# Optimization experiments

Hardware: AMD Instinct MI355X
Metric: run time of the kernel (lower is better)

The kernel has to match this reference:

```python
import jax, jax.numpy as jnp
import numpy as np

L, B, T, I, H, O = 2, 64, 256, 512, 1024, 256
HIDDEN_WEIGHT = 0.5  # placement_weight = 1 - hidden_weight
# dropout is identity in eval mode (reference is deterministic)


def setup_inputs() -> dict:
    key = jax.random.key(0)
    ks = jax.random.split(key, 20)
    def unif(k, shape, fan):
        b = 1.0 / np.sqrt(fan)
        return jax.random.uniform(k, shape, jnp.float32, -b, b)
    lengths = jax.random.randint(ks[4], (B,), 0, T + 1)
    lengths = lengths.at[0].set(T).at[1].set(0)  # exercise full-length and zero-length paths
    return {
        "step_input": jax.random.normal(ks[0], (B, T, I), jnp.float32),
        "clstm_hidden": jax.random.normal(ks[1], (B, H), jnp.float32),
        "hidden": jax.random.normal(ks[2], (L, B, H), jnp.float32),
        "cell": jax.random.normal(ks[3], (L, B, H), jnp.float32),
        "input_lengths": lengths.astype(jnp.int64),
        # LSTM params, PyTorch gate order [i, f, g, o]
        "w_ih0": unif(ks[5], (4 * H, I), H), "w_hh0": unif(ks[6], (4 * H, H), H),
        "b_ih0": unif(ks[7], (4 * H,), H), "b_hh0": unif(ks[8], (4 * H,), H),
        "w_ih1": unif(ks[9], (4 * H, H), H), "w_hh1": unif(ks[10], (4 * H, H), H),
        "b_ih1": unif(ks[11], (4 * H,), H), "b_hh1": unif(ks[12], (4 * H,), H),
        "w1": unif(ks[13], (H, H), H), "b1": unif(ks[14], (H,), H),
        "w2": unif(ks[15], (O, H), H), "b2": unif(ks[16], (O,), H),
    }


def compute_weighted_hidden(clstm_hidden, hidden, lens):
    # vectorized version of the per-(layer,batch) min-max rescale loop
    cmin = jnp.min(clstm_hidden, axis=-1, keepdims=True)            # [B,1]
    crange = jnp.max(clstm_hidden, axis=-1, keepdims=True) - cmin   # [B,1]
    safe_cr = jnp.where(crange > 0, crange, 1.0)
    s = jnp.where(crange > 0, (clstm_hidden - cmin) / safe_cr, clstm_hidden)  # [B,H]
    hmin = jnp.min(hidden, axis=-1, keepdims=True)                  # [L,B,1]
    hrange = jnp.max(hidden, axis=-1, keepdims=True) - hmin         # [L,B,1]
    s2 = jnp.where(hrange > 0, hmin + s[None] * hrange,
                   jnp.broadcast_to(s[None], hidden.shape))         # [L,B,H]
    c = jnp.where((lens == 0)[None, :, None], clstm_hidden[None], s2)
    return HIDDEN_WEIGHT * hidden + (1.0 - HIDDEN_WEIGHT) * c


def lstm_forward(x, h0, c0, lens, layer_params):
    # x: [B,T,I]; h0,c0: [L,B,H]; lens already clamped to >=1
    t_idx = jnp.arange(x.shape[1])

    def step(carry, xt_t):
        h, c = carry                      # each [L,B,H]
        xt, t = xt_t                      # xt: [B,I]
        valid = (t < lens)[:, None]       # [B,1]
        inp = xt
        hs, cs = [], []
        for l, (wih, whh, bih, bhh) in enumerate(layer_params):
            gates = inp @ wih.T + bih + h[l] @ whh.T + bhh   # [B,4H]
            i, f, g, o = jnp.split(gates, 4, axis=-1)
            i, f, o = jax.nn.sigmoid(i), jax.nn.sigmoid(f), jax.nn.sigmoid(o)
            g = jnp.tanh(g)
            c_new = f * c[l] + i * g
            h_new = o * jnp.tanh(c_new)
            hs.append(jnp.where(valid, h_new, h[l]))
            cs.append(jnp.where(valid, c_new, c[l]))
            inp = jnp.where(valid, h_new, 0.0)
        out_t = inp                        # top layer output, zeroed on padding
        return (jnp.stack(hs), jnp.stack(cs)), out_t

    (hn, cn), outs = jax.lax.scan(step, (h0, c0), (x.transpose(1, 0, 2), t_idx))
    return outs.transpose(1, 0, 2), hn, cn  # [B,T,H], [L,B,H], [L,B,H]


def reference(step_input, clstm_hidden, hidden, cell, input_lengths,
              w_ih0, w_hh0, b_ih0, b_hh0, w_ih1, w_hh1, b_ih1, b_hh1,
              w1, b1, w2, b2):
    weighted_hidden = compute_weighted_hidden(clstm_hidden, hidden, input_lengths)
    lens = jnp.clip(input_lengths, 1, None)  # torch.clamp(min=1)
    layer_params = [(w_ih0, w_hh0, b_ih0, b_hh0), (w_ih1, w_hh1, b_ih1, b_hh1)]
    lstm_out, hn, cn = lstm_forward(step_input, weighted_hidden, cell, lens, layer_params)
    # dropout layers are identity in eval mode
    h1 = jax.nn.relu(lstm_out @ w1.T + b1)
    logits = jax.nn.relu(h1 @ w2.T + b2)  # [B,T,O]
    zero = (input_lengths == 0)
    logits = jnp.where(zero[:, None, None], 0.0, logits)
    hn = jnp.where(zero[None, :, None], 0.0, hn)
    cn = jnp.where(zero[None, :, None], 0.0, cn)
    return logits, hn, cn
```

## Files before the change

### kernel.cpp

```cpp
#include <hip/hip_runtime.h>


typedef __bf16 bf16x8 __attribute__((ext_vector_type(8)));
typedef float f32x4 __attribute__((ext_vector_type(4)));
typedef int i32x4 __attribute__((ext_vector_type(4)));

__device__ __forceinline__ unsigned short f2bf(float f) {
  unsigned u = __float_as_uint(f);
  u = u + 0x7FFFu + ((u >> 16) & 1u);
  return (unsigned short)(u >> 16);
}
__device__ __forceinline__ float sigm_(float x) { return 1.f / (1.f + __expf(-x)); }
__device__ __forceinline__ float tanh_(float x) { return 1.f - 2.f / (__expf(2.f * x) + 1.f); }

__device__ __forceinline__ int hxoff(int b, int u) {
  return (b >> 4) * 16384 + (u >> 5) * 512 + ((u >> 3) & 3) * 128 + (b & 15) * 8 + (u & 7);
}

__global__ void cvt_kernel(const float* __restrict__ s, unsigned short* __restrict__ d, int n) {
  int i = (blockIdx.x * 256 + threadIdx.x) * 4;
  if (i < n) {
    float4 v = *reinterpret_cast<const float4*>(s + i);
    ushort4 o = make_ushort4(f2bf(v.x), f2bf(v.y), f2bf(v.z), f2bf(v.w));
    *reinterpret_cast<ushort4*>(d + i) = o;
  }
}

__global__ __launch_bounds__(256) void prep_kernel(
    const float* __restrict__ clstm, const float* __restrict__ hidden,
    const float* __restrict__ cell, const int* __restrict__ lens,
    float* __restrict__ hstate, float* __restrict__ cstate,
    unsigned short* __restrict__ h0buf, unsigned short* __restrict__ h1buf,
    const float* __restrict__ bih0, const float* __restrict__ bhh0,
    const float* __restrict__ bih1, const float* __restrict__ bhh1,
    float* __restrict__ bias0, float* __restrict__ bias1p,
    unsigned* __restrict__ bar) {
  const int tid = threadIdx.x, blk = blockIdx.x;
  const int l = blk >> 6, b = blk & 63;
  const float* crow = clstm + b * 1024;
  const float* hrow = hidden + ((size_t)l * 64 + b) * 1024;
  float cmn = 3.4e38f, cmx = -3.4e38f, hmn = 3.4e38f, hmx = -3.4e38f;
  for (int i = tid; i < 1024; i += 256) {
    float c = crow[i], h = hrow[i];
    cmn = fminf(cmn, c); cmx = fmaxf(cmx, c);
    hmn = fminf(hmn, h); hmx = fmaxf(hmx, h);
  }
#pragma unroll
  for (int off = 32; off > 0; off >>= 1) {
    cmn = fminf(cmn, __shfl_xor(cmn, off));
    cmx = fmaxf(cmx, __shfl_xor(cmx, off));
    hmn = fminf(hmn, __shfl_xor(hmn, off));
    hmx = fmaxf(hmx, __shfl_xor(hmx, off));
  }
  __shared__ float red[4][4];
  int wv = tid >> 6;
  if ((tid & 63) == 0) { red[wv][0] = cmn; red[wv][1] = cmx; red[wv][2] = hmn; red[wv][3] = hmx; }
  __syncthreads();
  cmn = fminf(fminf(red[0][0], red[1][0]), fminf(red[2][0], red[3][0]));
  cmx = fmaxf(fmaxf(red[0][1], red[1][1]), fmaxf(red[2][1], red[3][1]));
  hmn = fminf(fminf(red[0][2], red[1][2]), fminf(red[2][2], red[3][2]));
  hmx = fmaxf(fmaxf(red[0][3], red[1][3]), fmaxf(red[2][3], red[3][3]));
  const float crange = cmx - cmn, hrange = hmx - hmn;
  const int len = lens[b];
  const size_t base = ((size_t)l * 64 + b) * 1024;
  unsigned short* dst = (l == 0) ? h0buf : (h1buf + 65536);
  for (int i = tid; i < 1024; i += 256) {
    float cv = crow[i], hv = hrow[i];
    float s = (crange > 0.f) ? (cv - cmn) / crange : cv;
    float s2 = (hrange > 0.f) ? (hmn + s * hrange) : s;
    float cc = (len == 0) ? cv : s2;
    float w = 0.5f * hv + 0.5f * cc;
    hstate[base + i] = w;
    cstate[base + i] = cell[base + i];
    dst[hxoff(b, i)] = f2bf(w);
  }
  if (blk == 0) {
    for (int n = tid; n < 4096; n += 256) {
      bias0[n] = bih0[n] + bhh0[n];
      bias1p[(n & 1023) * 4 + (n >> 10)] = bih1[n] + bhh1[n];
    }
    bar[tid] = 0u; bar[256 + tid] = 0u;
  }
}

template <int AMODE, int EPI>
__global__ __launch_bounds__(256) void gemm_kernel(
    const void* __restrict__ Ap, const unsigned short* __restrict__ Bw,
    void* __restrict__ Cout, const float* __restrict__ bias,
    const int* __restrict__ lens, int M, int N, int K, int t0) {
  __shared__ unsigned short Al[128][40];
  __shared__ unsigned short Bl[128][40];
  const int tid = threadIdx.x;
  const int m0 = blockIdx.y * 128, n0 = blockIdx.x * 128;
  const int srow = tid >> 2;
  const int c8 = (tid & 3) * 8;
  size_t aoff0, aoff1;
  {
    int r = m0 + srow, r2 = r + 64;
    if (AMODE == 0) {
      aoff0 = (size_t)r * K; aoff1 = (size_t)r2 * K;
    } else {
      aoff0 = ((size_t)(r & 63) * 256 + t0 + (r >> 6)) * K;
      aoff1 = ((size_t)(r2 & 63) * 256 + t0 + (r2 >> 6)) * K;
    }
  }
  const size_t boff0 = (size_t)(n0 + srow) * K, boff1 = (size_t)(n0 + srow + 64) * K;
  const int wave = tid >> 6, lane = tid & 63, ln = lane & 15, quad = lane >> 4;
  const int mq = (wave >> 1) * 64, nq = (wave & 1) * 64;
  f32x4 acc[4][4] = {};
  const int nkt = K >> 5;
  for (int kt = 0; kt < nkt; ++kt) {
    const int kc = kt * 32 + c8;
    if (AMODE == 1) {
      const float* A = (const float*)Ap;
      const float* p0 = A + aoff0 + kc;
      const float* p1 = A + aoff1 + kc;
      float4 v0 = *reinterpret_cast<const float4*>(p0);
      float4 v0b = *reinterpret_cast<const float4*>(p0 + 4);
      float4 v1 = *reinterpret_cast<const float4*>(p1);
      float4 v1b = *reinterpret_cast<const float4*>(p1 + 4);
      *reinterpret_cast<ushort4*>(&Al[srow][c8]) =
          make_ushort4(f2bf(v0.x), f2bf(v0.y), f2bf(v0.z), f2bf(v0.w));
      *reinterpret_cast<ushort4*>(&Al[srow][c8 + 4]) =
          make_ushort4(f2bf(v0b.x), f2bf(v0b.y), f2bf(v0b.z), f2bf(v0b.w));
      *reinterpret_cast<ushort4*>(&Al[srow + 64][c8]) =
          make_ushort4(f2bf(v1.x), f2bf(v1.y), f2bf(v1.z), f2bf(v1.w));
      *reinterpret_cast<ushort4*>(&Al[srow + 64][c8 + 4]) =
          make_ushort4(f2bf(v1b.x), f2bf(v1b.y), f2bf(v1b.z), f2bf(v1b.w));
    } else {
      const unsigned short* A = (const unsigned short*)Ap;
      *reinterpret_cast<int4*>(&Al[srow][c8]) = *reinterpret_cast<const int4*>(A + aoff0 + kc);
      *reinterpret_cast<int4*>(&Al[srow + 64][c8]) = *reinterpret_cast<const int4*>(A + aoff1 + kc);
    }
    *reinterpret_cast<int4*>(&Bl[srow][c8]) = *reinterpret_cast<const int4*>(Bw + boff0 + kc);
    *reinterpret_cast<int4*>(&Bl[srow + 64][c8]) = *reinterpret_cast<const int4*>(Bw + boff1 + kc);
    __syncthreads();
    bf16x8 af[4], bfr[4];
#pragma unroll
    for (int i = 0; i < 4; ++i) {
      af[i] = *reinterpret_cast<const bf16x8*>(&Al[mq + i * 16 + ln][quad * 8]);
      bfr[i] = *reinterpret_cast<const bf16x8*>(&Bl[nq + i * 16 + ln][quad * 8]);
    }
#pragma unroll
    for (int i = 0; i < 4; ++i)
#pragma unroll
      for (int j = 0; j < 4; ++j)
        acc[i][j] = __builtin_amdgcn_mfma_f32_16x16x32_bf16(af[i], bfr[j], acc[i][j], 0, 0, 0);
    __syncthreads();
  }
#pragma unroll
  for (int i = 0; i < 4; ++i) {
    int mmb = m0 + mq + i * 16 + quad * 4;
#pragma unroll
    for (int j = 0; j < 4; ++j) {
      int nn = n0 + nq + j * 16 + ln;
      float bv = bias[nn];
#pragma unroll
      for (int r = 0; r < 4; ++r) {
        int mm = mmb + r;
        float v = acc[i][j][r] + bv;
        if (EPI >= 1) v = fmaxf(v, 0.f);
        if (EPI == 2) {
          if (lens[mm >> 8] == 0) v = 0.f;
          ((float*)Cout)[(size_t)mm * N + nn] = v;
        } else if (EPI == 1) {
          ((unsigned short*)Cout)[(size_t)mm * N + nn] = f2bf(v);
        } else {
          size_t idx = ((size_t)mm * 128 + ((nn >> 3) & 127)) * 32 + (nn & 7) * 4 + (nn >> 10);
          ((float*)Cout)[idx] = v;
        }
      }
    }
  }
}

#define HLo(dst, ptr, off) \
  asm volatile("global_load_dwordx4 %0, %1, off offset:" off " sc0 sc1" \
               : "=v"(dst) : "v"(ptr))
#define HL4(h0, h1, h2, h3, ptr) \
  HLo(h0, ptr, "0"); HLo(h1, ptr, "1024"); HLo(h2, ptr, "2048"); HLo(h3, ptr, "3072")
#define HLF(dst, ptr) \
  asm volatile("global_load_dwordx4 %0, %1, off sc0 sc1" : "=v"(dst) : "v"(ptr))
#define HST(ptr, val) \
  asm volatile("global_store_dwordx4 %0, %1, off sc0 sc1" :: "v"(ptr), "v"(val) : "memory")

__global__ __launch_bounds__(512) void rec2_kernel(
    const unsigned short* __restrict__ whh0b,
    const unsigned short* __restrict__ wih1b,
    const unsigned short* __restrict__ whh1b,
    const float* __restrict__ G2,
    const float* __restrict__ bias1p,
    unsigned short* __restrict__ h0buf,
    unsigned short* __restrict__ h1buf,
    float* __restrict__ pre1buf,
    float* __restrict__ hstate, float* __restrict__ cstate,
    unsigned short* __restrict__ h1out,
    const int* __restrict__ lens, int t0, int nint, unsigned* __restrict__ bar) {
  __shared__ unsigned short wlds[48 * 1032];
  __shared__ float glds[2][64][73];
  __shared__ unsigned short hsh[64][16];
  const int tid = threadIdx.x;
  const int bid = blockIdx.x;
  const bool isL1 = bid >= 128;
  const int g = bid & 127;
  {
    int r = tid >> 3;
    if (r < 48) {
      int c0 = (tid & 7) * 128;
      const unsigned short* src;
      if (!isL1) {
        if (r < 16)
          src = whh0b + (size_t)((2 + (r >> 3)) * 1024 + g * 8 + (r & 7)) * 1024;
        else {
          int c2 = r - 16;
          src = wih1b + (size_t)((c2 >> 3) * 1024 + g * 8 + (c2 & 7)) * 1024;
        }
      } else {
        src = whh1b + (size_t)((1 + (r >> 4)) * 1024 + g * 16 + (r & 15)) * 1024;
      }
      const i32x4* s4 = reinterpret_cast<const i32x4*>(src + c0);
      i32x4* dst = reinterpret_cast<i32x4*>(wlds + r * 1032 + c0);
#pragma unroll
      for (int j = 0; j < 16; ++j) dst[j] = s4[j];
    }
  }
  const int wave = tid >> 6, lane = tid & 63, ln = lane & 15, quad = lane >> 4;
  const int mt = wave & 3, kw = wave >> 2;
  bf16x8 breg[16];
  {
    const unsigned short* bp;
    if (!isL1)
      bp = whh0b + (size_t)((ln >> 3) * 1024 + g * 8 + (ln & 7)) * 1024 + kw * 512 + quad * 8;
    else
      bp = whh1b + (size_t)(g * 16 + ln) * 1024 + kw * 512 + quad * 8;
#pragma unroll
    for (int kt = 0; kt < 16; ++kt)
      breg[kt] = *reinterpret_cast<const bf16x8*>(bp + kt * 32);
  }
  const int b = tid >> 3, ul = tid & 7;
  const size_t sb0 = (size_t)(isL1 ? 65536 : 0) + (size_t)b * 1024 +
                     (isL1 ? g * 16 + ul : g * 8 + ul);
  float cm0 = cstate[sb0], hm0 = hstate[sb0];
  float cm1 = 0.f, hm1 = 0.f;
  if (isL1) { cm1 = cstate[sb0 + 8]; hm1 = hstate[sb0 + 8]; }
  int lv0 = lens[b];
  const int len = lv0 < 1 ? 1 : lv0;
  int lvA = lens[mt * 16 + ln];
  const int lenmA = lvA < 1 ? 1 : lvA;
  f32x4 b1a = {0.f, 0.f, 0.f, 0.f}, b1b = {0.f, 0.f, 0.f, 0.f};
  if (isL1) {
    b1a = *reinterpret_cast<const f32x4*>(bias1p + (g * 16 + ul) * 4);
    b1b = *reinterpret_cast<const f32x4*>(bias1p + (g * 16 + 8 + ul) * 4);
  }
  int lenp = 257;
  if (isL1 && tid < 128) { int lv = lens[tid >> 1]; lenp = lv < 1 ? 1 : lv; }
  const int puboff = (tid >> 4) * 16384 + (g >> 2) * 512 + (g & 3) * 128 + (tid & 15) * 8;
  const int pub1off = ((tid >> 1) >> 4) * 16384 + (g >> 1) * 512 +
                      ((g * 2 + (tid & 1)) & 3) * 128 + ((tid >> 1) & 15) * 8;
  const bf16x8 z8 = {};
  const i32x4 zi = {};
  __syncthreads();

  for (int k = 0; k < nint; ++k) {
    const int s = t0 + k;
    const bool actG = (!isL1) && (k < 64);
    const bool actP = (!isL1) && (s >= 1) && (s <= 256);
    const bool actL = isL1 && (s >= 2);
    if (actG || actP || actL) {
      bf16x8 hf[16];
      const unsigned short* p = (isL1 ? h1buf + ((s - 1) & 1) * 65536
                                      : h0buf + (s & 1) * 65536) +
                                mt * 16384 + kw * 8192 + lane * 8;
      HL4(hf[0], hf[1], hf[2], hf[3], p);
      HL4(hf[4], hf[5], hf[6], hf[7], p + 2048);
      HL4(hf[8], hf[9], hf[10], hf[11], p + 4096);
      HL4(hf[12], hf[13], hf[14], hf[15], p + 6144);
      f32x4 pga = {0.f, 0.f, 0.f, 0.f}, pgb = {0.f, 0.f, 0.f, 0.f};
      if (actG)
        pga = *reinterpret_cast<const f32x4*>(
            G2 + (((size_t)(k * 64 + b)) * 128 + g) * 32 + ul * 4);
      if (isL1) {
        const float* pr = pre1buf + (size_t)(s & 1) * 262144 +
                          ((size_t)b * 1024 + g * 16) * 4;
        HLF(pga, pr + ul * 4);
        HLF(pgb, pr + (8 + ul) * 4);
      }
      asm volatile("s_waitcnt vmcnt(0)" ::: "memory");
      __builtin_amdgcn_sched_barrier(0);
      const bool maskA = (!isL1) && ((s - 1) >= lenmA);
      f32x4 acc0 = {0.f, 0.f, 0.f, 0.f}, acc1 = acc0, acc2 = acc0, acc3 = acc0;
      const unsigned short* wp = wlds + ln * 1032 + kw * 512 + quad * 8;
#pragma unroll
      for (int kt = 0; kt < 16; ++kt) {
        const unsigned short* c = wp + kt * 32;
        bf16x8 bB = *reinterpret_cast<const bf16x8*>(c);
        bf16x8 bC = *reinterpret_cast<const bf16x8*>(c + 16512);
        bf16x8 bD = *reinterpret_cast<const bf16x8*>(c + 33024);
        bf16x8 a_ = hf[kt];
        acc0 = __builtin_amdgcn_mfma_f32_16x16x32_bf16(a_, breg[kt], acc0, 0, 0, 0);
        acc1 = __builtin_amdgcn_mfma_f32_16x16x32_bf16(a_, bB, acc1, 0, 0, 0);
        bf16x8 am = maskA ? z8 : a_;
        acc2 = __builtin_amdgcn_mfma_f32_16x16x32_bf16(am, bC, acc2, 0, 0, 0);
        acc3 = __builtin_amdgcn_mfma_f32_16x16x32_bf16(am, bD, acc3, 0, 0, 0);
      }
#pragma unroll
      for (int r = 0; r < 4; ++r) {
        float* gp = &glds[kw][mt * 16 + quad * 4 + r][0];
        gp[ln] = acc0[r]; gp[16 + ln] = acc1[r];
        gp[32 + ln] = acc2[r]; gp[48 + ln] = acc3[r];
      }
      __syncthreads();
      const float* g0 = &glds[0][b][0];
      const float* g1 = &glds[1][b][0];
      if (actG) {
        float pi = g0[ul] + g1[ul] + pga.x;
        float pf = g0[8 + ul] + g1[8 + ul] + pga.y;
        float pgg = g0[16 + ul] + g1[16 + ul] + pga.z;
        float po = g0[24 + ul] + g1[24 + ul] + pga.w;
        float ig = sigm_(pi), fg = sigm_(pf), gv = tanh_(pgg), og = sigm_(po);
        float cn_ = fg * cm0 + ig * gv;
        float hn_ = og * tanh_(cn_);
        if (s < len) { cm0 = cn_; hm0 = hn_; }
        hsh[b][ul] = f2bf(hm0);
      }
      if (actP) {
        f32x4 pv;
        pv.x = g0[32 + ul] + g1[32 + ul];
        pv.y = g0[40 + ul] + g1[40 + ul];
        pv.z = g0[48 + ul] + g1[48 + ul];
        pv.w = g0[56 + ul] + g1[56 + ul];
        float* pd = pre1buf + (size_t)((s - 1) & 1) * 262144 +
                    (size_t)b * 4096 + g * 32 + ul * 4;
        HST(pd, pv);
        asm volatile("s_waitcnt vmcnt(0)" ::: "memory");
      }
      if (actL) {
        {
          float pi = g0[ul] + g1[ul] + pga.x + b1a.x;
          float pf = g0[16 + ul] + g1[16 + ul] + pga.y + b1a.y;
          float pgg = g0[32 + ul] + g1[32 + ul] + pga.z + b1a.z;
          float po = g0[48 + ul] + g1[48 + ul] + pga.w + b1a.w;
          float ig = sigm_(pi), fg = sigm_(pf), gv = tanh_(pgg), og = sigm_(po);
          float cn_ = fg * cm0 + ig * gv;
          float hn_ = og * tanh_(cn_);
          if (s - 2 < len) { cm0 = cn_; hm0 = hn_; }
          hsh[b][ul] = f2bf(hm0);
        }
        {
          int iu = 8 + ul;
          float pi = g0[iu] + g1[iu] + pgb.x + b1b.x;
          float pf = g0[16 + iu] + g1[16 + iu] + pgb.y + b1b.y;
          float pgg = g0[32 + iu] + g1[32 + iu] + pgb.z + b1b.z;
          float po = g0[48 + iu] + g1[48 + iu] + pgb.w + b1b.w;
          float ig = sigm_(pi), fg = sigm_(pf), gv = tanh_(pgg), og = sigm_(po);
          float cn_ = fg * cm1 + ig * gv;
          float hn_ = og * tanh_(cn_);
          if (s - 2 < len) { cm1 = cn_; hm1 = hn_; }
          hsh[b][iu] = f2bf(hm1);
        }
      }
      __syncthreads();
      if (!isL1) {
        if (actG && tid < 64) {
          i32x4 v = *reinterpret_cast<const i32x4*>(&hsh[tid][0]);
          unsigned short* d = h0buf + ((s + 1) & 1) * 65536 + puboff;
          HST(d, v);
          asm volatile("s_waitcnt vmcnt(0)" ::: "memory");
        }
      } else {
        if (tid < 128) {
          const int pb = tid >> 1, half = tid & 1;
          i32x4 v = *reinterpret_cast<const i32x4*>(&hsh[pb][half * 8]);
          unsigned short* d = h1buf + (s & 1) * 65536 + pub1off;
          HST(d, v);
          const int t = s - 2;
          i32x4 vo = (t < lenp) ? v : zi;
          *reinterpret_cast<i32x4*>(h1out + ((size_t)pb * 256 + t) * 1024 +
                                    g * 16 + half * 8) = vo;
          asm volatile("s_waitcnt vmcnt(0)" ::: "memory");
        }
      }
    }
    __syncthreads();
    if (tid == 0) {
      unsigned a = __hip_atomic_fetch_add(bar + ((bid >> 4) << 4), 1u,
                                          __ATOMIC_RELAXED, __HIP_MEMORY_SCOPE_AGENT);
      if ((a & 15u) == 15u) {
        unsigned m = __hip_atomic_fetch_add(bar + 496, 1u,
                                            __ATOMIC_RELAXED, __HIP_MEMORY_SCOPE_AGENT);
        if ((m % 12u) == 11u) {
#pragma unroll
          for (int j = 0; j < 8; ++j)
            __hip_atomic_store(bar + 256 + (j << 4), m + 1u,
                               __ATOMIC_RELAXED, __HIP_MEMORY_SCOPE_AGENT);
        }
      }
      const unsigned tgt = 12u * (unsigned)(s + 1);
      while (__hip_atomic_load(bar + 256 + ((bid & 7) << 4),
                               __ATOMIC_RELAXED, __HIP_MEMORY_SCOPE_AGENT) < tgt)
        __builtin_amdgcn_s_sleep(2);
    }
    __syncthreads();
  }
  hstate[sb0] = hm0; cstate[sb0] = cm0;
  if (isL1) { hstate[sb0 + 8] = hm1; cstate[sb0 + 8] = cm1; }
}

__global__ void final_kernel(const float* __restrict__ hstate, const float* __restrict__ cstate,
                             const int* __restrict__ lens, float* __restrict__ out) {
  int i = blockIdx.x * 256 + threadIdx.x;
  int b = (i >> 10) & 63;
  float z = (lens[b] == 0) ? 0.f : 1.f;
  out[4194304 + i] = z * hstate[i];
  out[4325376 + i] = z * cstate[i];
}

extern "C" void kernel_launch(void* const* d_in, const int* in_sizes, int n_in,
                              void* d_out, int out_size, void* d_ws, size_t ws_size,
                              hipStream_t stream) {
  const float* x = (const float*)d_in[0];
  const float* clstm = (const float*)d_in[1];
  const float* hidden = (const float*)d_in[2];
  const float* cell = (const float*)d_in[3];
  const int* lens = (const int*)d_in[4];
  const float* wih0 = (const float*)d_in[5];
  const float* whh0 = (const float*)d_in[6];
  const float* bih0 = (const float*)d_in[7];
  const float* bhh0 = (const float*)d_in[8];
  const float* wih1 = (const float*)d_in[9];
  const float* whh1 = (const float*)d_in[10];
  const float* bih1 = (const float*)d_in[11];
  const float* bhh1 = (const float*)d_in[12];
  const float* w1 = (const float*)d_in[13];
  const float* b1 = (const float*)d_in[14];
  const float* w2 = (const float*)d_in[15];
  const float* b2 = (const float*)d_in[16];
  float* out = (float*)d_out;

  char* ws = (char*)d_ws;
  size_t off = 0;
  auto alloc = [&](size_t bytes) -> void* {
    void* p = ws + off;
    off += (bytes + 255) & ~(size_t)255;
    return p;
  };
  unsigned short* wih0_b = (unsigned short*)alloc(2097152ull * 2);
  unsigned short* whh0_b = (unsigned short*)alloc(4194304ull * 2);
  unsigned short* wih1_b = (unsigned short*)alloc(4194304ull * 2);
  unsigned short* whh1_b = (unsigned short*)alloc(4194304ull * 2);
  unsigned short* w1_b = (unsigned short*)alloc(1048576ull * 2);
  unsigned short* w2_b = (unsigned short*)alloc(262144ull * 2);
  float* bias0 = (float*)alloc(4096 * 4);
  float* bias1p = (float*)alloc(4096 * 4);
  float* hstate = (float*)alloc(131072ull * 4);
  float* cstate = (float*)alloc(131072ull * 4);
  unsigned short* h0buf = (unsigned short*)alloc(131072ull * 2);
  unsigned short* h1buf = (unsigned short*)alloc(131072ull * 2);
  float* pre1buf = (float*)alloc(524288ull * 4);
  unsigned* bar = (unsigned*)alloc(2048);
  float* G = (float*)alloc(16777216ull * 4);
  unsigned short* h1out = (unsigned short*)alloc(16777216ull * 2);

  cvt_kernel<<<2048, 256, 0, stream>>>(wih0, wih0_b, 2097152);
  cvt_kernel<<<4096, 256, 0, stream>>>(whh0, whh0_b, 4194304);
  cvt_kernel<<<4096, 256, 0, stream>>>(wih1, wih1_b, 4194304);
  cvt_kernel<<<4096, 256, 0, stream>>>(whh1, whh1_b, 4194304);
  cvt_kernel<<<1024, 256, 0, stream>>>(w1, w1_b, 1048576);
  cvt_kernel<<<256, 256, 0, stream>>>(w2, w2_b, 262144);

  prep_kernel<<<128, 256, 0, stream>>>(clstm, hidden, cell, lens, hstate, cstate,
                                       h0buf, h1buf, bih0, bhh0, bih1, bhh1,
                                       bias0, bias1p, bar);

  for (int c = 0; c < 4; ++c) {
    gemm_kernel<1, 0><<<dim3(32, 32), 256, 0, stream>>>(x, wih0_b, G, bias0, lens,
                                                        4096, 4096, 512, c * 64);
    rec2_kernel<<<192, 512, 0, stream>>>(whh0_b, wih1_b, whh1_b, G, bias1p,
                                         h0buf, h1buf, pre1buf, hstate, cstate,
                                         h1out, lens, c * 64, (c == 3) ? 66 : 64, bar);
  }
  gemm_kernel<0, 1><<<dim3(8, 128), 256, 0, stream>>>(h1out, w1_b, (void*)G, b1, lens,
                                                      16384, 1024, 1024, 0);
  gemm_kernel<0, 2><<<dim3(2, 128), 256, 0, stream>>>((const void*)G, w2_b, out, b2, lens,
                                                      16384, 256, 1024, 0);
  final_kernel<<<512, 256, 0, stream>>>(hstate, cstate, lens, out);
}
```

Before: 2.160 ms.

## Move second weight tile to registers and split h-load wait across k halves

Moves a second 16-row weight block from LDS into per-lane registers (bregB), which shrinks the LDS weight tile from 48 to 32 rows. The wait on the h-state loads is split: the first half of the MFMA k-loop starts after vmcnt(8), so it overlaps the remaining loads. The pre1 loads are issued first, and several store waits are relaxed or merged. This raises register pressure by 16 bf16x8 vectors per lane and makes correctness depend on the exact vmcnt ordering of the loads.

```diff
diff --git a/kernel.cpp b/kernel.cpp
--- a/kernel.cpp
+++ b/kernel.cpp
@@ -196,7 +196,7 @@
     float* __restrict__ hstate, float* __restrict__ cstate,
     unsigned short* __restrict__ h1out,
     const int* __restrict__ lens, int t0, int nint, unsigned* __restrict__ bar) {
-  __shared__ unsigned short wlds[48 * 1032];
+  __shared__ unsigned short wlds[32 * 1032];
   __shared__ float glds[2][64][73];
   __shared__ unsigned short hsh[64][16];
   const int tid = threadIdx.x;
@@ -204,38 +204,35 @@
   const bool isL1 = bid >= 128;
   const int g = bid & 127;
   {
-    int r = tid >> 3;
-    if (r < 48) {
-      int c0 = (tid & 7) * 128;
-      const unsigned short* src;
-      if (!isL1) {
-        if (r < 16)
-          src = whh0b + (size_t)((2 + (r >> 3)) * 1024 + g * 8 + (r & 7)) * 1024;
-        else {
-          int c2 = r - 16;
-          src = wih1b + (size_t)((c2 >> 3) * 1024 + g * 8 + (c2 & 7)) * 1024;
-        }
-      } else {
-        src = whh1b + (size_t)((1 + (r >> 4)) * 1024 + g * 16 + (r & 15)) * 1024;
-      }
-      const i32x4* s4 = reinterpret_cast<const i32x4*>(src + c0);
-      i32x4* dst = reinterpret_cast<i32x4*>(wlds + r * 1032 + c0);
-#pragma unroll
-      for (int j = 0; j < 16; ++j) dst[j] = s4[j];
-    }
+    int r = tid >> 4;
+    int c0 = (tid & 15) * 64;
+    const unsigned short* src;
+    if (!isL1)
+      src = wih1b + (size_t)((r >> 3) * 1024 + g * 8 + (r & 7)) * 1024;
+    else
+      src = whh1b + (size_t)((2 + (r >> 4)) * 1024 + g * 16 + (r & 15)) * 1024;
+    const i32x4* s4 = reinterpret_cast<const i32x4*>(src + c0);
+    i32x4* dst = reinterpret_cast<i32x4*>(wlds + r * 1032 + c0);
+#pragma unroll
+    for (int j = 0; j < 8; ++j) dst[j] = s4[j];
   }
   const int wave = tid >> 6, lane = tid & 63, ln = lane & 15, quad = lane >> 4;
   const int mt = wave & 3, kw = wave >> 2;
-  bf16x8 breg[16];
+  bf16x8 bregA[16], bregB[16];
   {
-    const unsigned short* bp;
-    if (!isL1)
-      bp = whh0b + (size_t)((ln >> 3) * 1024 + g * 8 + (ln & 7)) * 1024 + kw * 512 + quad * 8;
-    else
-      bp = whh1b + (size_t)(g * 16 + ln) * 1024 + kw * 512 + quad * 8;
-#pragma unroll
-    for (int kt = 0; kt < 16; ++kt)
-      breg[kt] = *reinterpret_cast<const bf16x8*>(bp + kt * 32);
+    const unsigned short *bpA, *bpB;
+    if (!isL1) {
+      bpA = whh0b + (size_t)((ln >> 3) * 1024 + g * 8 + (ln & 7)) * 1024 + kw * 512 + quad * 8;
+      bpB = whh0b + (size_t)((2 + (ln >> 3)) * 1024 + g * 8 + (ln & 7)) * 1024 + kw * 512 + quad * 8;
+    } else {
+      bpA = whh1b + (size_t)(g * 16 + ln) * 1024 + kw * 512 + quad * 8;
+      bpB = whh1b + (size_t)(1024 + g * 16 + ln) * 1024 + kw * 512 + quad * 8;
+    }
+#pragma unroll
+    for (int kt = 0; kt < 16; ++kt) {
+      bregA[kt] = *reinterpret_cast<const bf16x8*>(bpA + kt * 32);
+      bregB[kt] = *reinterpret_cast<const bf16x8*>(bpB + kt * 32);
+    }
   }
   const int b = tid >> 3, ul = tid & 7;
   const size_t sb0 = (size_t)(isL1 ? 65536 : 0) + (size_t)b * 1024 +
@@ -267,6 +264,13 @@
     const bool actP = (!isL1) && (s >= 1) && (s <= 256);
     const bool actL = isL1 && (s >= 2);
     if (actG || actP || actL) {
+      f32x4 pga = {0.f, 0.f, 0.f, 0.f}, pgb = {0.f, 0.f, 0.f, 0.f};
+      if (isL1) {
+        const float* pr = pre1buf + (size_t)(s & 1) * 262144 +
+                          ((size_t)b * 1024 + g * 16) * 4;
+        HLF(pga, pr + ul * 4);
+        HLF(pgb, pr + (8 + ul) * 4);
+      }
       bf16x8 hf[16];
       const unsigned short* p = (isL1 ? h1buf + ((s - 1) & 1) * 65536
                                       : h0buf + (s & 1) * 65536) +
@@ -275,30 +279,36 @@
       HL4(hf[4], hf[5], hf[6], hf[7], p + 2048);
       HL4(hf[8], hf[9], hf[10], hf[11], p + 4096);
       HL4(hf[12], hf[13], hf[14], hf[15], p + 6144);
-      f32x4 pga = {0.f, 0.f, 0.f, 0.f}, pgb = {0.f, 0.f, 0.f, 0.f};
       if (actG)
         pga = *reinterpret_cast<const f32x4*>(
             G2 + (((size_t)(k * 64 + b)) * 128 + g) * 32 + ul * 4);
-      if (isL1) {
-        const float* pr = pre1buf + (size_t)(s & 1) * 262144 +
-                          ((size_t)b * 1024 + g * 16) * 4;
-        HLF(pga, pr + ul * 4);
-        HLF(pgb, pr + (8 + ul) * 4);
-      }
-      asm volatile("s_waitcnt vmcnt(0)" ::: "memory");
-      __builtin_amdgcn_sched_barrier(0);
       const bool maskA = (!isL1) && ((s - 1) >= lenmA);
       f32x4 acc0 = {0.f, 0.f, 0.f, 0.f}, acc1 = acc0, acc2 = acc0, acc3 = acc0;
       const unsigned short* wp = wlds + ln * 1032 + kw * 512 + quad * 8;
-#pragma unroll
-      for (int kt = 0; kt < 16; ++kt) {
+      asm volatile("s_waitcnt vmcnt(8)" ::: "memory");
+      __builtin_amdgcn_sched_barrier(0);
+#pragma unroll
+      for (int kt = 0; kt < 8; ++kt) {
         const unsigned short* c = wp + kt * 32;
-        bf16x8 bB = *reinterpret_cast<const bf16x8*>(c);
-        bf16x8 bC = *reinterpret_cast<const bf16x8*>(c + 16512);
-        bf16x8 bD = *reinterpret_cast<const bf16x8*>(c + 33024);
+        bf16x8 bC = *reinterpret_cast<const bf16x8*>(c);
+        bf16x8 bD = *reinterpret_cast<const bf16x8*>(c + 16512);
         bf16x8 a_ = hf[kt];
-        acc0 = __builtin_amdgcn_mfma_f32_16x16x32_bf16(a_, breg[kt], acc0, 0, 0, 0);
-        acc1 = __builtin_amdgcn_mfma_f32_16x16x32_bf16(a_, bB, acc1, 0, 0, 0);
+        acc0 = __builtin_amdgcn_mfma_f32_16x16x32_bf16(a_, bregA[kt], acc0, 0, 0, 0);
+        acc1 = __builtin_amdgcn_mfma_f32_16x16x32_bf16(a_, bregB[kt], acc1, 0, 0, 0);
+        bf16x8 am = maskA ? z8 : a_;
+        acc2 = __builtin_amdgcn_mfma_f32_16x16x32_bf16(am, bC, acc2, 0, 0, 0);
+        acc3 = __builtin_amdgcn_mfma_f32_16x16x32_bf16(am, bD, acc3, 0, 0, 0);
+      }
+      asm volatile("s_waitcnt vmcnt(0)" ::: "memory");
+      __builtin_amdgcn_sched_barrier(0);
+#pragma unroll
+      for (int kt = 8; kt < 16; ++kt) {
+        const unsigned short* c = wp + kt * 32;
+        bf16x8 bC = *reinterpret_cast<const bf16x8*>(c);
+        bf16x8 bD = *reinterpret_cast<const bf16x8*>(c + 16512);
+        bf16x8 a_ = hf[kt];
+        acc0 = __builtin_amdgcn_mfma_f32_16x16x32_bf16(a_, bregA[kt], acc0, 0, 0, 0);
+        acc1 = __builtin_amdgcn_mfma_f32_16x16x32_bf16(a_, bregB[kt], acc1, 0, 0, 0);
         bf16x8 am = maskA ? z8 : a_;
         acc2 = __builtin_amdgcn_mfma_f32_16x16x32_bf16(am, bC, acc2, 0, 0, 0);
         acc3 = __builtin_amdgcn_mfma_f32_16x16x32_bf16(am, bD, acc3, 0, 0, 0);
@@ -332,7 +342,6 @@
         float* pd = pre1buf + (size_t)((s - 1) & 1) * 262144 +
                     (size_t)b * 4096 + g * 32 + ul * 4;
         HST(pd, pv);
-        asm volatile("s_waitcnt vmcnt(0)" ::: "memory");
       }
       if (actL) {
         {
@@ -365,8 +374,8 @@
           i32x4 v = *reinterpret_cast<const i32x4*>(&hsh[tid][0]);
           unsigned short* d = h0buf + ((s + 1) & 1) * 65536 + puboff;
           HST(d, v);
-          asm volatile("s_waitcnt vmcnt(0)" ::: "memory");
-        }
+        }
+        asm volatile("s_waitcnt vmcnt(0)" ::: "memory");
       } else {
         if (tid < 128) {
           const int pb = tid >> 1, half = tid & 1;
@@ -377,7 +386,7 @@
           i32x4 vo = (t < lenp) ? v : zi;
           *reinterpret_cast<i32x4*>(h1out + ((size_t)pb * 256 + t) * 1024 +
                                     g * 16 + half * 8) = vo;
-          asm volatile("s_waitcnt vmcnt(0)" ::: "memory");
+          asm volatile("s_waitcnt vmcnt(1)" ::: "memory");
         }
       }
     }
```

Measured after the change: 2.062 ms. -4.5%, faster.
